# Optimization experiments

Hardware: AMD Instinct MI355X
Metric: run time of the kernel (lower is better)

Reference implementation:

```python
import jax, jax.numpy as jnp
import numpy as np

EMBED_DIM = 1024
NUM_HEADS = 16
HEAD_DIM = EMBED_DIM // NUM_HEADS
SCALE = HEAD_DIM ** -0.5
B, S = 2, 2048


def setup_inputs() -> dict:
    key = jax.random.key(0)
    ks = jax.random.split(key, 10)
    def lin(kw, kb, fan_in):
        bound = 1.0 / np.sqrt(fan_in)
        W = jax.random.uniform(kw, (EMBED_DIM, EMBED_DIM), jnp.float32, -bound, bound)
        b = jax.random.uniform(kb, (EMBED_DIM,), jnp.float32, -bound, bound)
        return W, b
    Wq, bq = lin(ks[0], ks[1], EMBED_DIM)
    Wk, bk = lin(ks[2], ks[3], EMBED_DIM)
    Wv, bv = lin(ks[4], ks[5], EMBED_DIM)
    Wo, bo = lin(ks[6], ks[7], EMBED_DIM)
    x = jax.random.normal(ks[8], (B, S, EMBED_DIM), jnp.float32)
    # sparsity_mask: True where token kept (rand > sparsity with sparsity=0.5)
    sparsity_mask = jax.random.randint(ks[9], (B, NUM_HEADS, S), 0, 2).astype(bool)
    return {"x": x, "sparsity_mask": sparsity_mask,
            "Wq": Wq, "bq": bq, "Wk": Wk, "bk": bk,
            "Wv": Wv, "bv": bv, "Wo": Wo, "bo": bo}


def reference(x, sparsity_mask, Wq, bq, Wk, bk, Wv, bv, Wo, bo):
    b, s, _ = x.shape
    def heads(W, bias):
        # torch Linear: x @ W.T + b ; then [b, s, h, d] -> [b, h, s, d]
        y = x @ W.T + bias
        return y.reshape(b, s, NUM_HEADS, HEAD_DIM).transpose(0, 2, 1, 3)
    q = heads(Wq, bq)
    k = heads(Wk, bk)
    v = heads(Wv, bv)
    m = sparsity_mask[..., None].astype(q.dtype)  # [b, h, s, 1]
    q = q * m
    k = k * m
    attn = jnp.einsum('bhqd,bhkd->bhqk', q, k) * SCALE
    attn = jax.nn.softmax(attn, axis=-1)
    out = jnp.einsum('bhqk,bhkd->bhqd', attn, v)
    out = out.transpose(0, 2, 1, 3).reshape(b, s, EMBED_DIM)
    return out @ Wo.T + bo
```

## Files before the change

### kernel.cpp

```cpp
#include <hip/hip_runtime.h>

#define DEV __device__ __forceinline__

typedef __bf16 bf16x8 __attribute__((ext_vector_type(8)));
typedef __bf16 bf16x4 __attribute__((ext_vector_type(4)));
typedef float f32x4 __attribute__((ext_vector_type(4)));
typedef unsigned u32x4 __attribute__((ext_vector_type(4)));
typedef unsigned short ushort_t;

static constexpr int EMBED = 1024;
static constexpr int NHEAD = 16;
static constexpr int HDIM  = 64;
static constexpr int S_    = 2048;
static constexpr float SCALE_L2E = 0.125f * 1.44269504088896340736f;

DEV ushort_t f2bf(float f) {
  unsigned u = __builtin_bit_cast(unsigned, f);
  unsigned r = (u + 0x7fffu + ((u >> 16) & 1u)) >> 16;
  return (ushort_t)r;
}

#define GLOAD_LDS16(g, l)                                                   \
  __builtin_amdgcn_global_load_lds(                                         \
      (const __attribute__((address_space(1))) unsigned int*)(g),           \
      (__attribute__((address_space(3))) unsigned int*)(l), 16, 0, 0)

#define DRAIN_VM() asm volatile("s_waitcnt vmcnt(0)" ::: "memory")

__global__ __launch_bounds__(256) void convert_kernel(
    const float* __restrict__ x,
    const float* __restrict__ wq, const float* __restrict__ wk,
    const float* __restrict__ wv, const float* __restrict__ wo,
    ushort_t* __restrict__ xb, ushort_t* __restrict__ wqb,
    ushort_t* __restrict__ wkb, ushort_t* __restrict__ wvb,
    ushort_t* __restrict__ wob) {
  size_t i = ((size_t)blockIdx.x * blockDim.x + threadIdx.x) * 4;
  const float* src; ushort_t* dst; size_t off;
  if (i < 4194304u)      { src = x;  dst = xb;  off = i; }
  else if (i < 5242880u) { src = wq; dst = wqb; off = i - 4194304u; }
  else if (i < 6291456u) { src = wk; dst = wkb; off = i - 5242880u; }
  else if (i < 7340032u) { src = wv; dst = wvb; off = i - 6291456u; }
  else                   { src = wo; dst = wob; off = i - 7340032u; }
  float4 v = *(const float4*)(src + off);
  ushort4 o;
  o.x = f2bf(v.x); o.y = f2bf(v.y); o.z = f2bf(v.z); o.w = f2bf(v.w);
  *(ushort4*)(dst + off) = o;
}

__global__ __launch_bounds__(256) void qkv_kernel(
    const ushort_t* __restrict__ xb, const ushort_t* __restrict__ wqb,
    const ushort_t* __restrict__ wkb, const ushort_t* __restrict__ wvb,
    const float* __restrict__ bq, const float* __restrict__ bk,
    const float* __restrict__ bv, const int* __restrict__ mask,
    ushort_t* __restrict__ qo, ushort_t* __restrict__ ko,
    ushort_t* __restrict__ vto) {
  __shared__ __align__(16) unsigned char ldsA[16384];
  __shared__ __align__(16) unsigned char ldsB[16384];
  __shared__ float maskf[2][128];

  const int bid  = blockIdx.x;
  const int tid  = threadIdx.x;
  const int lane = tid & 63;
  const int w    = tid >> 6;
  const int wm   = (w >> 1) * 64;
  const int wn   = (w & 1) * 64;
  const int rl   = lane & 15;
  const int kg   = lane >> 4;

  int mode, ar0, br0;
  const ushort_t *A, *Bm;
  const float* bias;
  if (bid < 512) {
    mode = bid >> 8;
    int t = bid & 255;
    ar0 = (t & 31) * 128;
    br0 = (t >> 5) * 128;
    A = xb; Bm = mode ? wkb : wqb; bias = mode ? bk : bq;
  } else {
    mode = 2;
    int t = bid - 512;
    ar0 = (t & 7) * 128;
    br0 = (t >> 3) * 128;
    A = wvb; Bm = xb; bias = bv;
  }

  if (mode < 2) {
    int hl = tid >> 7, sl = tid & 127;
    int m = ar0 + sl;
    int b = m >> 11, s = m & 2047;
    int h = (br0 >> 6) + hl;
    maskf[hl][sl] = (float)mask[((size_t)b * NHEAD + h) * S_ + s];
  }

  f32x4 acc[4][4];
#pragma unroll
  for (int i = 0; i < 4; ++i)
#pragma unroll
    for (int j = 0; j < 4; ++j) acc[i][j] = f32x4{0.f, 0.f, 0.f, 0.f};

  auto STAGE = [&](int kt) {
    const int k0 = kt * 64;
#pragma unroll
    for (int s = 0; s < 8; ++s) {
      const int basev = s * 256 + w * 64;
      const int Lb = basev & 1023;
      const int L = Lb + lane;
      const int row = L >> 3;
      const int gu = (L & 7) ^ (row & 7);
      if (s < 4) {
        GLOAD_LDS16(A + (size_t)(ar0 + row) * EMBED + k0 + gu * 8, &ldsA[Lb * 16]);
      } else {
        GLOAD_LDS16(Bm + (size_t)(br0 + row) * EMBED + k0 + gu * 8, &ldsB[Lb * 16]);
      }
    }
  };

  for (int kt = 0; kt < 16; ++kt) {
    if (kt) __syncthreads();
    STAGE(kt);
    DRAIN_VM();
    __syncthreads();
#pragma unroll
    for (int kk = 0; kk < 2; ++kk) {
      bf16x8 af[4], bfr[4];
#pragma unroll
      for (int mb = 0; mb < 4; ++mb) {
        const int row = wm + mb * 16 + rl;
        const int off = (kk * 64 + kg * 16) ^ ((row & 7) << 4);
        af[mb] = *(const bf16x8*)(ldsA + row * 128 + off);
      }
#pragma unroll
      for (int nb = 0; nb < 4; ++nb) {
        const int row = wn + nb * 16 + rl;
        const int off = (kk * 64 + kg * 16) ^ ((row & 7) << 4);
        bfr[nb] = *(const bf16x8*)(ldsB + row * 128 + off);
      }
#pragma unroll
      for (int mb = 0; mb < 4; ++mb)
#pragma unroll
        for (int nb = 0; nb < 4; ++nb)
          acc[mb][nb] = __builtin_amdgcn_mfma_f32_16x16x32_bf16(
              af[mb], bfr[nb], acc[mb][nb], 0, 0, 0);
    }
  }

#pragma unroll
  for (int mb = 0; mb < 4; ++mb)
#pragma unroll
    for (int nb = 0; nb < 4; ++nb)
#pragma unroll
      for (int r = 0; r < 4; ++r) {
        int row_l = wm + mb * 16 + kg * 4 + r;
        int col_l = wn + nb * 16 + rl;
        float v = acc[mb][nb][r];
        if (mode < 2) {
          int m = ar0 + row_l, n = br0 + col_l;
          v = (v + bias[n]) * maskf[col_l >> 6][row_l];
          if (mode == 0) v *= SCALE_L2E;
          int b = m >> 11, s = m & 2047, h = n >> 6, d = n & 63;
          ushort_t* o = mode ? ko : qo;
          o[(((size_t)(b * NHEAD + h)) * S_ + s) * HDIM + d] = f2bf(v);
        } else {
          int n = ar0 + row_l, m = br0 + col_l;
          v += bias[n];
          int b = m >> 11, s = m & 2047, h = n >> 6, d = n & 63;
          vto[(((size_t)(b * NHEAD + h)) * HDIM + d) * S_ + s] = f2bf(v);
        }
      }
}

__global__ __launch_bounds__(256) void gemm_o_kernel(
    const ushort_t* __restrict__ A, const ushort_t* __restrict__ Bm,
    const float* __restrict__ bias, float* __restrict__ outp) {
  __shared__ __align__(16) unsigned char ldsA[16384];
  __shared__ __align__(16) unsigned char ldsB[16384];

  const int tid  = threadIdx.x;
  const int lane = tid & 63;
  const int w    = tid >> 6;
  const int ar0  = blockIdx.x * 128;
  const int br0  = blockIdx.y * 128;
  const int wm   = (w >> 1) * 64;
  const int wn   = (w & 1) * 64;
  const int rl   = lane & 15;
  const int kg   = lane >> 4;

  f32x4 acc[4][4];
#pragma unroll
  for (int i = 0; i < 4; ++i)
#pragma unroll
    for (int j = 0; j < 4; ++j) acc[i][j] = f32x4{0.f, 0.f, 0.f, 0.f};

  auto STAGE = [&](int kt) {
    const int k0 = kt * 64;
#pragma unroll
    for (int s = 0; s < 8; ++s) {
      const int basev = s * 256 + w * 64;
      const int Lb = basev & 1023;
      const int L = Lb + lane;
      const int row = L >> 3;
      const int gu = (L & 7) ^ (row & 7);
      if (s < 4) {
        GLOAD_LDS16(A + (size_t)(ar0 + row) * EMBED + k0 + gu * 8, &ldsA[Lb * 16]);
      } else {
        GLOAD_LDS16(Bm + (size_t)(br0 + row) * EMBED + k0 + gu * 8, &ldsB[Lb * 16]);
      }
    }
  };

  for (int kt = 0; kt < 16; ++kt) {
    if (kt) __syncthreads();
    STAGE(kt);
    DRAIN_VM();
    __syncthreads();
#pragma unroll
    for (int kk = 0; kk < 2; ++kk) {
      bf16x8 af[4], bfr[4];
#pragma unroll
      for (int mb = 0; mb < 4; ++mb) {
        const int row = wm + mb * 16 + rl;
        const int off = (kk * 64 + kg * 16) ^ ((row & 7) << 4);
        af[mb] = *(const bf16x8*)(ldsA + row * 128 + off);
      }
#pragma unroll
      for (int nb = 0; nb < 4; ++nb) {
        const int row = wn + nb * 16 + rl;
        const int off = (kk * 64 + kg * 16) ^ ((row & 7) << 4);
        bfr[nb] = *(const bf16x8*)(ldsB + row * 128 + off);
      }
#pragma unroll
      for (int mb = 0; mb < 4; ++mb)
#pragma unroll
        for (int nb = 0; nb < 4; ++nb)
          acc[mb][nb] = __builtin_amdgcn_mfma_f32_16x16x32_bf16(
              af[mb], bfr[nb], acc[mb][nb], 0, 0, 0);
    }
  }

#pragma unroll
  for (int mb = 0; mb < 4; ++mb)
#pragma unroll
    for (int nb = 0; nb < 4; ++nb)
#pragma unroll
      for (int r = 0; r < 4; ++r) {
        int m = ar0 + wm + mb * 16 + kg * 4 + r;
        int n = br0 + wn + nb * 16 + rl;
        outp[(size_t)m * EMBED + n] = acc[mb][nb][r] + bias[n];
      }
}

__global__ __launch_bounds__(512) void attn_kernel(
    const ushort_t* __restrict__ qp, const ushort_t* __restrict__ kp,
    const ushort_t* __restrict__ vtp, ushort_t* __restrict__ ao) {
  __shared__ __align__(16) unsigned char ldsK[4][8192];
  __shared__ __align__(16) unsigned char ldsV[4][8192];
  __shared__ __align__(16) unsigned char ldsP[8][2048];

  const int bid  = blockIdx.x;
  const int bh   = (bid & 7) * 4 + (bid >> 7);
  const int qt   = (bid >> 3) & 15;
  const int tid  = threadIdx.x;
  const int lane = tid & 63;
  const int w    = tid >> 6;
  const int q0   = qt * 128 + w * 16;
  const int rl   = lane & 15;
  const int kg   = lane >> 4;
  const int pswz = (rl & 7) << 4;

  const bf16x8 ones = __builtin_bit_cast(bf16x8,
      u32x4{0x3F803F80u, 0x3F803F80u, 0x3F803F80u, 0x3F803F80u});

  bf16x8 qa[2];
#pragma unroll
  for (int kk = 0; kk < 2; ++kk)
    qa[kk] = *(const bf16x8*)(qp + ((size_t)bh * S_ + q0 + rl) * HDIM +
                              kk * 32 + kg * 8);

  f32x4 o_acc[4];
  f32x4 o_l = f32x4{0.f, 0.f, 0.f, 0.f};
#pragma unroll
  for (int nb = 0; nb < 4; ++nb) o_acc[nb] = f32x4{0.f, 0.f, 0.f, 0.f};

  unsigned char* pb = ldsP[w];

  auto STAGE = [&](int kt, int slot) {
#pragma unroll
    for (int s = 0; s < 2; ++s) {
      const int Lb = w * 64;
      const int L = Lb + lane;
      const int row = L >> 3;
      const int gu = (L & 7) ^ (row & 7);
      if (s == 0) {
        GLOAD_LDS16(kp + ((size_t)bh * S_ + (size_t)kt * 64 + row) * HDIM + gu * 8,
                    &ldsK[slot][L * 16]);
      } else {
        GLOAD_LDS16(vtp + ((size_t)bh * HDIM + row) * S_ + (size_t)kt * 64 + gu * 8,
                    &ldsV[slot][L * 16]);
      }
    }
  };

  auto QK = [&](int slot, f32x4 sa[4]) {
#pragma unroll
    for (int nb = 0; nb < 4; ++nb) {
      const int row = nb * 16 + rl;
#pragma unroll
      for (int kk = 0; kk < 2; ++kk) {
        bf16x8 kf = *(const bf16x8*)(ldsK[slot] + row * 128 +
                                     ((kk * 64 + kg * 16) ^ ((row & 7) << 4)));
        sa[nb] = __builtin_amdgcn_mfma_f32_16x16x32_bf16(kf, qa[kk], sa[nb], 0, 0, 0);
      }
    }
  };
  auto SMW = [&](const f32x4 sa[4]) {
#pragma unroll
    for (int nb = 0; nb < 4; ++nb) {
      bf16x4 pk4;
#pragma unroll
      for (int r = 0; r < 4; ++r)
        pk4[r] = (__bf16)__builtin_amdgcn_exp2f(sa[nb][r]);
      *(bf16x4*)(pb + rl * 128 + ((nb * 32 + kg * 8) ^ pswz)) = pk4;
    }
  };
  auto PVL = [&](int slot) {
    bf16x8 pa[2];
#pragma unroll
    for (int kk = 0; kk < 2; ++kk)
      pa[kk] = *(const bf16x8*)(pb + rl * 128 + ((kk * 64 + kg * 16) ^ pswz));
    o_l = __builtin_amdgcn_mfma_f32_16x16x32_bf16(pa[0], ones, o_l, 0, 0, 0);
    o_l = __builtin_amdgcn_mfma_f32_16x16x32_bf16(pa[1], ones, o_l, 0, 0, 0);
#pragma unroll
    for (int nb = 0; nb < 4; ++nb) {
      const int row = nb * 16 + rl;
#pragma unroll
      for (int kk = 0; kk < 2; ++kk) {
        bf16x8 vb = *(const bf16x8*)(ldsV[slot] + row * 128 +
                                     ((kk * 64 + kg * 16) ^ ((row & 7) << 4)));
        o_acc[nb] = __builtin_amdgcn_mfma_f32_16x16x32_bf16(pa[kk], vb, o_acc[nb], 0, 0, 0);
      }
    }
  };

  STAGE(0, 0); STAGE(1, 1); STAGE(2, 2); STAGE(3, 3);
  asm volatile("s_waitcnt vmcnt(4) lgkmcnt(0)" ::: "memory");
  __builtin_amdgcn_s_barrier();

  for (int kt = 0; kt < 32; kt += 2) {
    const int s0 = kt & 3, s1 = (kt + 1) & 3;

    f32x4 saA[4], saB[4];
#pragma unroll
    for (int nb = 0; nb < 4; ++nb) { saA[nb] = f32x4{0.f,0.f,0.f,0.f}; saB[nb] = f32x4{0.f,0.f,0.f,0.f}; }

    __builtin_amdgcn_s_setprio(1);
    QK(s0, saA);
    QK(s1, saB);
    __builtin_amdgcn_s_setprio(0);

    SMW(saA);
    asm volatile("s_waitcnt lgkmcnt(0)" ::: "memory");
    __builtin_amdgcn_sched_barrier(0);

    __builtin_amdgcn_s_setprio(1);
    PVL(s0);
    __builtin_amdgcn_s_setprio(0);
    SMW(saB);
    asm volatile("s_waitcnt lgkmcnt(0)" ::: "memory");
    __builtin_amdgcn_sched_barrier(0);

    __builtin_amdgcn_s_setprio(1);
    PVL(s1);
    __builtin_amdgcn_s_setprio(0);

    __builtin_amdgcn_s_barrier();
    if (kt + 4 < 32) {
      STAGE(kt + 4, s0); STAGE(kt + 5, s1);
      asm volatile("s_waitcnt vmcnt(4) lgkmcnt(0)" ::: "memory");
    } else {
      asm volatile("s_waitcnt vmcnt(0) lgkmcnt(0)" ::: "memory");
    }
    __builtin_amdgcn_s_barrier();
  }

  const int b = bh >> 4, h = bh & 15;
#pragma unroll
  for (int r = 0; r < 4; ++r) {
    float linv = 1.0f / o_l[r];
    const int row = q0 + kg * 4 + r;
#pragma unroll
    for (int nb = 0; nb < 4; ++nb) {
      float v = o_acc[nb][r] * linv;
      ao[((size_t)b * S_ + row) * EMBED + h * HDIM + nb * 16 + rl] = f2bf(v);
    }
  }
}

extern "C" void kernel_launch(void* const* d_in, const int* in_sizes, int n_in,
                              void* d_out, int out_size, void* d_ws, size_t ws_size,
                              hipStream_t stream) {
  const float* x    = (const float*)d_in[0];
  const int*   mask = (const int*)d_in[1];
  const float* Wq   = (const float*)d_in[2];
  const float* bq   = (const float*)d_in[3];
  const float* Wk   = (const float*)d_in[4];
  const float* bk   = (const float*)d_in[5];
  const float* Wv   = (const float*)d_in[6];
  const float* bv   = (const float*)d_in[7];
  const float* Wo   = (const float*)d_in[8];
  const float* bo   = (const float*)d_in[9];

  char* ws = (char*)d_ws;
  ushort_t* xb  = (ushort_t*)(ws);
  ushort_t* wqb = (ushort_t*)(ws + 8388608);
  ushort_t* wkb = (ushort_t*)(ws + 10485760);
  ushort_t* wvb = (ushort_t*)(ws + 12582912);
  ushort_t* wob = (ushort_t*)(ws + 14680064);
  ushort_t* qb  = (ushort_t*)(ws + 16777216);
  ushort_t* kb  = (ushort_t*)(ws + 25165824);
  ushort_t* vtb = (ushort_t*)(ws + 33554432);
  ushort_t* aob = (ushort_t*)(ws + 41943040);

  hipLaunchKernelGGL(convert_kernel, dim3(8192), dim3(256), 0, stream,
                     x, Wq, Wk, Wv, Wo, xb, wqb, wkb, wvb, wob);
  hipLaunchKernelGGL(qkv_kernel, dim3(768), dim3(256), 0, stream,
                     xb, wqb, wkb, wvb, bq, bk, bv, mask, qb, kb, vtb);
  hipLaunchKernelGGL(attn_kernel, dim3(512), dim3(512), 0, stream,
                     qb, kb, vtb, aob);
  hipLaunchKernelGGL(gemm_o_kernel, dim3(32, 8), dim3(256), 0, stream,
                     aob, wob, bo, (float*)d_out);
}
```

Before: 111.4 us.

## Load V tiles directly into registers instead of staging through LDS

```diff
diff --git a/kernel.cpp b/kernel.cpp
--- a/kernel.cpp
+++ b/kernel.cpp
@@ -249,11 +249,10 @@
       }
 }
 
-__global__ __launch_bounds__(512) void attn_kernel(
+__global__ __launch_bounds__(512, 4) void attn_kernel(
     const ushort_t* __restrict__ qp, const ushort_t* __restrict__ kp,
     const ushort_t* __restrict__ vtp, ushort_t* __restrict__ ao) {
   __shared__ __align__(16) unsigned char ldsK[4][8192];
-  __shared__ __align__(16) unsigned char ldsV[4][8192];
   __shared__ __align__(16) unsigned char ldsP[8][2048];
 
   const int bid  = blockIdx.x;
@@ -282,22 +281,24 @@
   for (int nb = 0; nb < 4; ++nb) o_acc[nb] = f32x4{0.f, 0.f, 0.f, 0.f};
 
   unsigned char* pb = ldsP[w];
+  const ushort_t* vbp = vtp + (size_t)bh * HDIM * S_;
 
   auto STAGE = [&](int kt, int slot) {
-#pragma unroll
-    for (int s = 0; s < 2; ++s) {
-      const int Lb = w * 64;
-      const int L = Lb + lane;
-      const int row = L >> 3;
-      const int gu = (L & 7) ^ (row & 7);
-      if (s == 0) {
-        GLOAD_LDS16(kp + ((size_t)bh * S_ + (size_t)kt * 64 + row) * HDIM + gu * 8,
-                    &ldsK[slot][L * 16]);
-      } else {
-        GLOAD_LDS16(vtp + ((size_t)bh * HDIM + row) * S_ + (size_t)kt * 64 + gu * 8,
-                    &ldsV[slot][L * 16]);
-      }
-    }
+    const int Lb = w * 64;
+    const int L = Lb + lane;
+    const int row = L >> 3;
+    const int gu = (L & 7) ^ (row & 7);
+    GLOAD_LDS16(kp + ((size_t)bh * S_ + (size_t)kt * 64 + row) * HDIM + gu * 8,
+                &ldsK[slot][L * 16]);
+  };
+
+  auto VLOAD = [&](int kt, bf16x8 vf[4][2]) {
+#pragma unroll
+    for (int nb = 0; nb < 4; ++nb)
+#pragma unroll
+      for (int kk = 0; kk < 2; ++kk)
+        vf[nb][kk] = *(const bf16x8*)(vbp + (size_t)(nb * 16 + rl) * S_ +
+                                      kt * 64 + kk * 32 + kg * 8);
   };
 
   auto QK = [&](int slot, f32x4 sa[4]) {
@@ -322,7 +323,7 @@
       *(bf16x4*)(pb + rl * 128 + ((nb * 32 + kg * 8) ^ pswz)) = pk4;
     }
   };
-  auto PVL = [&](int slot) {
+  auto PVL = [&](const bf16x8 vf[4][2]) {
     bf16x8 pa[2];
 #pragma unroll
     for (int kk = 0; kk < 2; ++kk)
@@ -330,23 +331,22 @@
     o_l = __builtin_amdgcn_mfma_f32_16x16x32_bf16(pa[0], ones, o_l, 0, 0, 0);
     o_l = __builtin_amdgcn_mfma_f32_16x16x32_bf16(pa[1], ones, o_l, 0, 0, 0);
 #pragma unroll
-    for (int nb = 0; nb < 4; ++nb) {
-      const int row = nb * 16 + rl;
-#pragma unroll
-      for (int kk = 0; kk < 2; ++kk) {
-        bf16x8 vb = *(const bf16x8*)(ldsV[slot] + row * 128 +
-                                     ((kk * 64 + kg * 16) ^ ((row & 7) << 4)));
-        o_acc[nb] = __builtin_amdgcn_mfma_f32_16x16x32_bf16(pa[kk], vb, o_acc[nb], 0, 0, 0);
-      }
-    }
+    for (int nb = 0; nb < 4; ++nb)
+#pragma unroll
+      for (int kk = 0; kk < 2; ++kk)
+        o_acc[nb] = __builtin_amdgcn_mfma_f32_16x16x32_bf16(pa[kk], vf[nb][kk], o_acc[nb], 0, 0, 0);
   };
 
   STAGE(0, 0); STAGE(1, 1); STAGE(2, 2); STAGE(3, 3);
-  asm volatile("s_waitcnt vmcnt(4) lgkmcnt(0)" ::: "memory");
+  asm volatile("s_waitcnt vmcnt(2) lgkmcnt(0)" ::: "memory");
   __builtin_amdgcn_s_barrier();
 
   for (int kt = 0; kt < 32; kt += 2) {
     const int s0 = kt & 3, s1 = (kt + 1) & 3;
+
+    bf16x8 vfA[4][2], vfB[4][2];
+    VLOAD(kt, vfA);
+    VLOAD(kt + 1, vfB);
 
     f32x4 saA[4], saB[4];
 #pragma unroll
@@ -362,20 +362,20 @@
     __builtin_amdgcn_sched_barrier(0);
 
     __builtin_amdgcn_s_setprio(1);
-    PVL(s0);
+    PVL(vfA);
     __builtin_amdgcn_s_setprio(0);
     SMW(saB);
     asm volatile("s_waitcnt lgkmcnt(0)" ::: "memory");
     __builtin_amdgcn_sched_barrier(0);
 
     __builtin_amdgcn_s_setprio(1);
-    PVL(s1);
+    PVL(vfB);
     __builtin_amdgcn_s_setprio(0);
 
     __builtin_amdgcn_s_barrier();
     if (kt + 4 < 32) {
       STAGE(kt + 4, s0); STAGE(kt + 5, s1);
-      asm volatile("s_waitcnt vmcnt(4) lgkmcnt(0)" ::: "memory");
+      asm volatile("s_waitcnt vmcnt(2) lgkmcnt(0)" ::: "memory");
     } else {
       asm volatile("s_waitcnt vmcnt(0) lgkmcnt(0)" ::: "memory");
     }
```

Result: slower. 231.6 us (+107.9%).

## Compute Q and K projections in one block sharing the staged x tile

Applied to the files above, without the earlier changes.

```diff
diff --git a/kernel.cpp b/kernel.cpp
--- a/kernel.cpp
+++ b/kernel.cpp
@@ -55,7 +55,8 @@
     ushort_t* __restrict__ qo, ushort_t* __restrict__ ko,
     ushort_t* __restrict__ vto) {
   __shared__ __align__(16) unsigned char ldsA[16384];
-  __shared__ __align__(16) unsigned char ldsB[16384];
+  __shared__ __align__(16) unsigned char ldsB0[16384];
+  __shared__ __align__(16) unsigned char ldsB1[16384];
   __shared__ float maskf[2][128];
 
   const int bid  = blockIdx.x;
@@ -67,106 +68,164 @@
   const int rl   = lane & 15;
   const int kg   = lane >> 4;
 
-  int mode, ar0, br0;
-  const ushort_t *A, *Bm;
-  const float* bias;
-  if (bid < 512) {
-    mode = bid >> 8;
-    int t = bid & 255;
-    ar0 = (t & 31) * 128;
-    br0 = (t >> 5) * 128;
-    A = xb; Bm = mode ? wkb : wqb; bias = mode ? bk : bq;
+  if (bid < 256) {
+    const int t   = bid;
+    const int ar0 = (t & 31) * 128;
+    const int br0 = (t >> 5) * 128;
+
+    {
+      int hl = tid >> 7, sl = tid & 127;
+      int m = ar0 + sl;
+      int b = m >> 11, s = m & 2047;
+      int h = (br0 >> 6) + hl;
+      maskf[hl][sl] = (float)mask[((size_t)b * NHEAD + h) * S_ + s];
+    }
+
+    f32x4 accQ[4][4], accK[4][4];
+#pragma unroll
+    for (int i = 0; i < 4; ++i)
+#pragma unroll
+      for (int j = 0; j < 4; ++j) {
+        accQ[i][j] = f32x4{0.f, 0.f, 0.f, 0.f};
+        accK[i][j] = f32x4{0.f, 0.f, 0.f, 0.f};
+      }
+
+    auto STAGE = [&](int kt) {
+      const int k0 = kt * 64;
+#pragma unroll
+      for (int s = 0; s < 12; ++s) {
+        const int Lb = (s & 3) * 256 + w * 64;
+        const int L = Lb + lane;
+        const int row = L >> 3;
+        const int gu = (L & 7) ^ (row & 7);
+        if (s < 4) {
+          GLOAD_LDS16(xb + (size_t)(ar0 + row) * EMBED + k0 + gu * 8, &ldsA[Lb * 16]);
+        } else if (s < 8) {
+          GLOAD_LDS16(wqb + (size_t)(br0 + row) * EMBED + k0 + gu * 8, &ldsB0[Lb * 16]);
+        } else {
+          GLOAD_LDS16(wkb + (size_t)(br0 + row) * EMBED + k0 + gu * 8, &ldsB1[Lb * 16]);
+        }
+      }
+    };
+
+    for (int kt = 0; kt < 16; ++kt) {
+      if (kt) __syncthreads();
+      STAGE(kt);
+      DRAIN_VM();
+      __syncthreads();
+#pragma unroll
+      for (int kk = 0; kk < 2; ++kk) {
+        bf16x8 af[4], bq4[4], bk4[4];
+#pragma unroll
+        for (int mb = 0; mb < 4; ++mb) {
+          const int row = wm + mb * 16 + rl;
+          const int off = (kk * 64 + kg * 16) ^ ((row & 7) << 4);
+          af[mb] = *(const bf16x8*)(ldsA + row * 128 + off);
+        }
+#pragma unroll
+        for (int nb = 0; nb < 4; ++nb) {
+          const int row = wn + nb * 16 + rl;
+          const int off = (kk * 64 + kg * 16) ^ ((row & 7) << 4);
+          bq4[nb] = *(const bf16x8*)(ldsB0 + row * 128 + off);
+          bk4[nb] = *(const bf16x8*)(ldsB1 + row * 128 + off);
+        }
+#pragma unroll
+        for (int mb = 0; mb < 4; ++mb)
+#pragma unroll
+          for (int nb = 0; nb < 4; ++nb) {
+            accQ[mb][nb] = __builtin_amdgcn_mfma_f32_16x16x32_bf16(
+                af[mb], bq4[nb], accQ[mb][nb], 0, 0, 0);
+            accK[mb][nb] = __builtin_amdgcn_mfma_f32_16x16x32_bf16(
+                af[mb], bk4[nb], accK[mb][nb], 0, 0, 0);
+          }
+      }
+    }
+
+#pragma unroll
+    for (int mb = 0; mb < 4; ++mb)
+#pragma unroll
+      for (int nb = 0; nb < 4; ++nb)
+#pragma unroll
+        for (int r = 0; r < 4; ++r) {
+          int row_l = wm + mb * 16 + kg * 4 + r;
+          int col_l = wn + nb * 16 + rl;
+          int m = ar0 + row_l, n = br0 + col_l;
+          float mk = maskf[col_l >> 6][row_l];
+          int b = m >> 11, s = m & 2047, h = n >> 6, d = n & 63;
+          size_t oidx = (((size_t)(b * NHEAD + h)) * S_ + s) * HDIM + d;
+          qo[oidx] = f2bf((accQ[mb][nb][r] + bq[n]) * mk * SCALE_L2E);
+          ko[oidx] = f2bf((accK[mb][nb][r] + bk[n]) * mk);
+        }
   } else {
-    mode = 2;
-    int t = bid - 512;
-    ar0 = (t & 7) * 128;
-    br0 = (t >> 3) * 128;
-    A = wvb; Bm = xb; bias = bv;
-  }
-
-  if (mode < 2) {
-    int hl = tid >> 7, sl = tid & 127;
-    int m = ar0 + sl;
-    int b = m >> 11, s = m & 2047;
-    int h = (br0 >> 6) + hl;
-    maskf[hl][sl] = (float)mask[((size_t)b * NHEAD + h) * S_ + s];
-  }
-
-  f32x4 acc[4][4];
-#pragma unroll
-  for (int i = 0; i < 4; ++i)
-#pragma unroll
-    for (int j = 0; j < 4; ++j) acc[i][j] = f32x4{0.f, 0.f, 0.f, 0.f};
-
-  auto STAGE = [&](int kt) {
-    const int k0 = kt * 64;
-#pragma unroll
-    for (int s = 0; s < 8; ++s) {
-      const int basev = s * 256 + w * 64;
-      const int Lb = basev & 1023;
-      const int L = Lb + lane;
-      const int row = L >> 3;
-      const int gu = (L & 7) ^ (row & 7);
-      if (s < 4) {
-        GLOAD_LDS16(A + (size_t)(ar0 + row) * EMBED + k0 + gu * 8, &ldsA[Lb * 16]);
-      } else {
-        GLOAD_LDS16(Bm + (size_t)(br0 + row) * EMBED + k0 + gu * 8, &ldsB[Lb * 16]);
-      }
-    }
-  };
-
-  for (int kt = 0; kt < 16; ++kt) {
-    if (kt) __syncthreads();
-    STAGE(kt);
-    DRAIN_VM();
-    __syncthreads();
-#pragma unroll
-    for (int kk = 0; kk < 2; ++kk) {
-      bf16x8 af[4], bfr[4];
-#pragma unroll
-      for (int mb = 0; mb < 4; ++mb) {
-        const int row = wm + mb * 16 + rl;
-        const int off = (kk * 64 + kg * 16) ^ ((row & 7) << 4);
-        af[mb] = *(const bf16x8*)(ldsA + row * 128 + off);
-      }
-#pragma unroll
-      for (int nb = 0; nb < 4; ++nb) {
-        const int row = wn + nb * 16 + rl;
-        const int off = (kk * 64 + kg * 16) ^ ((row & 7) << 4);
-        bfr[nb] = *(const bf16x8*)(ldsB + row * 128 + off);
-      }
-#pragma unroll
-      for (int mb = 0; mb < 4; ++mb)
-#pragma unroll
-        for (int nb = 0; nb < 4; ++nb)
-          acc[mb][nb] = __builtin_amdgcn_mfma_f32_16x16x32_bf16(
-              af[mb], bfr[nb], acc[mb][nb], 0, 0, 0);
-    }
-  }
-
-#pragma unroll
-  for (int mb = 0; mb < 4; ++mb)
-#pragma unroll
-    for (int nb = 0; nb < 4; ++nb)
-#pragma unroll
-      for (int r = 0; r < 4; ++r) {
-        int row_l = wm + mb * 16 + kg * 4 + r;
-        int col_l = wn + nb * 16 + rl;
-        float v = acc[mb][nb][r];
-        if (mode < 2) {
-          int m = ar0 + row_l, n = br0 + col_l;
-          v = (v + bias[n]) * maskf[col_l >> 6][row_l];
-          if (mode == 0) v *= SCALE_L2E;
-          int b = m >> 11, s = m & 2047, h = n >> 6, d = n & 63;
-          ushort_t* o = mode ? ko : qo;
-          o[(((size_t)(b * NHEAD + h)) * S_ + s) * HDIM + d] = f2bf(v);
+    const int t   = bid - 256;
+    const int ar0 = (t & 7) * 128;
+    const int br0 = (t >> 3) * 128;
+
+    f32x4 acc[4][4];
+#pragma unroll
+    for (int i = 0; i < 4; ++i)
+#pragma unroll
+      for (int j = 0; j < 4; ++j) acc[i][j] = f32x4{0.f, 0.f, 0.f, 0.f};
+
+    auto STAGE = [&](int kt) {
+      const int k0 = kt * 64;
+#pragma unroll
+      for (int s = 0; s < 8; ++s) {
+        const int Lb = (s & 3) * 256 + w * 64;
+        const int L = Lb + lane;
+        const int row = L >> 3;
+        const int gu = (L & 7) ^ (row & 7);
+        if (s < 4) {
+          GLOAD_LDS16(wvb + (size_t)(ar0 + row) * EMBED + k0 + gu * 8, &ldsA[Lb * 16]);
         } else {
+          GLOAD_LDS16(xb + (size_t)(br0 + row) * EMBED + k0 + gu * 8, &ldsB0[Lb * 16]);
+        }
+      }
+    };
+
+    for (int kt = 0; kt < 16; ++kt) {
+      if (kt) __syncthreads();
+      STAGE(kt);
+      DRAIN_VM();
+      __syncthreads();
+#pragma unroll
+      for (int kk = 0; kk < 2; ++kk) {
+        bf16x8 af[4], bfr[4];
+#pragma unroll
+        for (int mb = 0; mb < 4; ++mb) {
+          const int row = wm + mb * 16 + rl;
+          const int off = (kk * 64 + kg * 16) ^ ((row & 7) << 4);
+          af[mb] = *(const bf16x8*)(ldsA + row * 128 + off);
+        }
+#pragma unroll
+        for (int nb = 0; nb < 4; ++nb) {
+          const int row = wn + nb * 16 + rl;
+          const int off = (kk * 64 + kg * 16) ^ ((row & 7) << 4);
+          bfr[nb] = *(const bf16x8*)(ldsB0 + row * 128 + off);
+        }
+#pragma unroll
+        for (int mb = 0; mb < 4; ++mb)
+#pragma unroll
+          for (int nb = 0; nb < 4; ++nb)
+            acc[mb][nb] = __builtin_amdgcn_mfma_f32_16x16x32_bf16(
+                af[mb], bfr[nb], acc[mb][nb], 0, 0, 0);
+      }
+    }
+
+#pragma unroll
+    for (int mb = 0; mb < 4; ++mb)
+#pragma unroll
+      for (int nb = 0; nb < 4; ++nb)
+#pragma unroll
+        for (int r = 0; r < 4; ++r) {
+          int row_l = wm + mb * 16 + kg * 4 + r;
+          int col_l = wn + nb * 16 + rl;
           int n = ar0 + row_l, m = br0 + col_l;
-          v += bias[n];
+          float v = acc[mb][nb][r] + bv[n];
           int b = m >> 11, s = m & 2047, h = n >> 6, d = n & 63;
           vto[(((size_t)(b * NHEAD + h)) * HDIM + d) * S_ + s] = f2bf(v);
         }
-      }
+  }
 }
 
 __global__ __launch_bounds__(256) void gemm_o_kernel(
@@ -422,7 +481,7 @@
 
   hipLaunchKernelGGL(convert_kernel, dim3(8192), dim3(256), 0, stream,
                      x, Wq, Wk, Wv, Wo, xb, wqb, wkb, wvb, wob);
-  hipLaunchKernelGGL(qkv_kernel, dim3(768), dim3(256), 0, stream,
+  hipLaunchKernelGGL(qkv_kernel, dim3(512), dim3(256), 0, stream,
                      xb, wqb, wkb, wvb, bq, bk, bv, mask, qb, kb, vtb);
   hipLaunchKernelGGL(attn_kernel, dim3(512), dim3(512), 0, stream,
                      qb, kb, vtb, aob);
```

Result: slower. 116.4 us (+4.5%).
